# Kernel tuning notes

Hardware: AMD Instinct MI355X
Metric: run time of the kernel (lower is better)

Reference implementation:

```python
import jax, jax.numpy as jnp
import numpy as np

B, CIN, IMG = 8, 512, 112
P = IMG // 14          # patch_size = 8
NP = 14 * 14           # n_patch = 196
DEC, SKIP, EMB = 512, 512, 768
BN_EPS = 1e-3          # keras BatchNormalization default
IN_EPS = 1e-3          # tfa InstanceNormalization default


def conv2d(x, w, b, stride=1):
    # x: NCHW, w: OIHW
    y = jax.lax.conv_general_dilated(x, w, (stride, stride), 'VALID',
                                     dimension_numbers=('NCHW', 'OIHW', 'NCHW'))
    return y + b[None, :, None, None]


def bn_inf(x, g, b, m, v):
    scale = g / jnp.sqrt(v + BN_EPS)
    return (x - m[None, :, None, None]) * scale[None, :, None, None] + b[None, :, None, None]


def setup_inputs() -> dict:
    key = jax.random.key(0)
    ks = jax.random.split(key, 20)
    s = 0.05
    return {
        'decoder': jax.random.normal(ks[0], (B, CIN, IMG, IMG), jnp.float32),
        'trans': jax.random.normal(ks[1], (B, NP, EMB), jnp.float32),
        'pe_w': jax.random.normal(ks[2], (DEC, CIN, P, P), jnp.float32) * s,
        'pe_b': jax.random.normal(ks[3], (DEC,), jnp.float32) * s,
        'mc_w': jax.random.normal(ks[4], (SKIP, CIN, 1, 1), jnp.float32) * s,
        'mc_b': jax.random.normal(ks[5], (SKIP,), jnp.float32) * s,
        'bn1_g': jax.random.uniform(ks[6], (SKIP,), jnp.float32, 0.5, 1.5),
        'bn1_b': jax.random.normal(ks[7], (SKIP,), jnp.float32) * s,
        'bn1_m': jax.random.normal(ks[8], (SKIP,), jnp.float32) * s,
        'bn1_v': jax.random.uniform(ks[9], (SKIP,), jnp.float32, 0.5, 1.5),
        'wq': jax.random.normal(ks[10], (DEC, SKIP), jnp.float32) * s,
        'wk': jax.random.normal(ks[11], (EMB, SKIP), jnp.float32) * s,
        'wv': jax.random.normal(ks[12], (EMB, SKIP), jnp.float32) * s,
        'wo': jax.random.normal(ks[13], (SKIP, SKIP), jnp.float32) * s,
        'psi_g': jnp.ones((1,), jnp.float32),
        'psi_b': jnp.zeros((1,), jnp.float32),
        'rc_w': jax.random.normal(ks[14], (SKIP, SKIP, 1, 1), jnp.float32) * s,
        'rc_b': jax.random.normal(ks[15], (SKIP,), jnp.float32) * s,
        'bn2_g': jax.random.uniform(ks[16], (SKIP,), jnp.float32, 0.5, 1.5),
        'bn2_b': jax.random.normal(ks[17], (SKIP,), jnp.float32) * s,
        'bn2_m': jax.random.normal(ks[18], (SKIP,), jnp.float32) * s,
        'bn2_v': jax.random.uniform(ks[19], (SKIP,), jnp.float32, 0.5, 1.5),
    }


def reference(decoder, trans, pe_w, pe_b, mc_w, mc_b, bn1_g, bn1_b, bn1_m, bn1_v,
              wq, wk, wv, wo, psi_g, psi_b, rc_w, rc_b, bn2_g, bn2_b, bn2_m, bn2_v):
    # mask branch: 1x1 conv + BN + ReLU  -> [B, SKIP, IMG, IMG]
    mask = jax.nn.relu(bn_inf(conv2d(decoder, mc_w, mc_b), bn1_g, bn1_b, bn1_m, bn1_v))

    # patch embedding: strided conv -> [B, DEC, 14, 14] -> tokens [B, NP, DEC]
    dl = conv2d(decoder, pe_w, pe_b, stride=P)
    dl = dl.reshape(dl.shape[0], dl.shape[1], -1).transpose(0, 2, 1)

    q = jnp.einsum('bnd,ds->bsn', dl, wq)       # [B, SKIP, NP]
    k = jnp.einsum('bne,es->bns', trans, wk)    # [B, NP, SKIP]
    v = jnp.einsum('bne,es->bsn', trans, wv)    # [B, SKIP, NP]

    sim = jnp.einsum('bsn,bnt->bst', q, k)      # [B, SKIP, SKIP]
    # InstanceNorm over the (SKIP, SKIP) map per sample (single channel)
    mu = sim.mean(axis=(1, 2), keepdims=True)
    var = sim.var(axis=(1, 2), keepdims=True)
    sim = (sim - mu) / jnp.sqrt(var + IN_EPS) * psi_g[0] + psi_b[0]
    sim = jax.nn.softmax(sim, axis=-1)

    out = jnp.einsum('bst,btn->bns', sim, v)    # [B, NP, SKIP]
    out = jnp.einsum('bns,so->bno', out, wo)    # [B, NP, SKIP]

    # reconstruct: tokens -> [B, SKIP, 14, 14] -> nearest upsample x P -> 1x1 conv + BN + ReLU
    x = out.transpose(0, 2, 1).reshape(out.shape[0], SKIP, 14, 14)
    x = jnp.repeat(jnp.repeat(x, P, axis=2), P, axis=3)
    x = jax.nn.relu(bn_inf(conv2d(x, rc_w, rc_b), bn2_g, bn2_b, bn2_m, bn2_v))

    return x * mask
```

## Files before the change

kernel.cpp:

```cpp
#include <hip/hip_runtime.h>
#include <stdint.h>

typedef __attribute__((ext_vector_type(8))) short v8s;
typedef __attribute__((ext_vector_type(4))) float v4f;

__device__ __forceinline__ uint16_t f2bf(float x){
  uint32_t u = __float_as_uint(x);
  return (uint16_t)((u + 0x7FFFu + ((u >> 16) & 1u)) >> 16);
}
__device__ __forceinline__ uint32_t pk2(float a, float b){
  return (uint32_t)f2bf(a) | ((uint32_t)f2bf(b) << 16);
}

__device__ __forceinline__ void gl16(const uint16_t* g, uint16_t* l){
  __builtin_amdgcn_global_load_lds((const __attribute__((address_space(1))) void*)g,
                                   (__attribute__((address_space(3))) void*)l, 16, 0, 0);
}

__global__ void __launch_bounds__(256) dra_cvt(const float* __restrict__ s,
                                               uint16_t* __restrict__ d, int n8){
  int i = blockIdx.x * 256 + threadIdx.x;
  if (i >= n8) return;
  const float4* sp = (const float4*)(s + (size_t)i * 8);
  float4 f0 = sp[0], f1 = sp[1];
  uint4 u; u.x = pk2(f0.x, f0.y); u.y = pk2(f0.z, f0.w);
  u.z = pk2(f1.x, f1.y); u.w = pk2(f1.z, f1.w);
  *(uint4*)(d + (size_t)i * 8) = u;
}

__global__ void __launch_bounds__(256) dra_tcvt(const float* __restrict__ s,
                                                uint16_t* __restrict__ d, int R, int C){
  int r8 = R >> 3;
  int id = blockIdx.x * 256 + threadIdx.x;
  if (id >= C * r8) return;
  int c = id / r8, r0 = (id - c * r8) * 8;
  float v[8];
  #pragma unroll
  for (int e = 0; e < 8; e++) v[e] = s[(size_t)(r0 + e) * C + c];
  uint4 u; u.x = pk2(v[0], v[1]); u.y = pk2(v[2], v[3]);
  u.z = pk2(v[4], v[5]); u.w = pk2(v[6], v[7]);
  *(uint4*)(d + (size_t)c * R + r0) = u;
}

__global__ void __launch_bounds__(256) dra_tdec(const float* __restrict__ dec,
                                                uint16_t* __restrict__ decT){
  __shared__ uint16_t lt[64 * 80];
  int t = threadIdx.x;
  int pos0 = blockIdx.x * 64;
  int ci0  = blockIdx.y * 64;
  int b    = blockIdx.z;
  #pragma unroll
  for (int i = 0; i < 4; i++){
    int idx = t + i * 256;
    int ci_l = idx >> 4, p4 = (idx & 15) * 4;
    const float4 f = *(const float4*)(dec + ((size_t)(b * 512 + ci0 + ci_l)) * 12544 + pos0 + p4);
    lt[(p4 + 0) * 80 + ci_l] = f2bf(f.x);
    lt[(p4 + 1) * 80 + ci_l] = f2bf(f.y);
    lt[(p4 + 2) * 80 + ci_l] = f2bf(f.z);
    lt[(p4 + 3) * 80 + ci_l] = f2bf(f.w);
  }
  __syncthreads();
  #pragma unroll
  for (int i = 0; i < 2; i++){
    int idx = t + i * 256;
    int p_l = idx >> 3, u = idx & 7;
    uint4 v = *(const uint4*)&lt[p_l * 80 + u * 8];
    *(uint4*)(decT + ((size_t)b * 12544 + pos0 + p_l) * 512 + ci0 + u * 8) = v;
  }
}

__global__ void __launch_bounds__(256) dra_wpe2(const float* __restrict__ pw,
                                                uint16_t* __restrict__ w2){
  int id = blockIdx.x * 256 + threadIdx.x;
  if (id >= 2097152) return;
  int co = id >> 12, rem = id & 4095;
  int ci8 = rem >> 6, pix = rem & 63;
  const float* s = pw + (size_t)co * 32768 + ci8 * 512 + pix;
  float v[8];
  #pragma unroll
  for (int j = 0; j < 8; j++) v[j] = s[j * 64];
  uint4 u; u.x = pk2(v[0], v[1]); u.y = pk2(v[2], v[3]);
  u.z = pk2(v[4], v[5]); u.w = pk2(v[6], v[7]);
  *(uint4*)(w2 + (size_t)co * 32768 + pix * 512 + ci8 * 8) = u;
}

__global__ void __launch_bounds__(256) dra_transb(const float* __restrict__ tr,
                                                  uint16_t* __restrict__ d){
  int id = blockIdx.x * 256 + threadIdx.x;
  if (id >= 1792 * 96) return;
  int n = id / 96, e0 = (id - n * 96) * 8;
  int b = n / 224, nl = n - b * 224;
  uint4 u = {0u,0u,0u,0u};
  if (nl < 196){
    const float* sp = tr + ((size_t)(b * 196 + nl)) * 768 + e0;
    u.x = pk2(sp[0], sp[1]); u.y = pk2(sp[2], sp[3]);
    u.z = pk2(sp[4], sp[5]); u.w = pk2(sp[6], sp[7]);
  }
  *(uint4*)(d + (size_t)n * 768 + e0) = u;
}

__global__ void dra_scales(const float* mcb, const float* g1, const float* b1,
                           const float* m1, const float* v1,
                           const float* rcb, const float* g2, const float* b2,
                           const float* m2, const float* v2,
                           float* s1, float* o1, float* s2, float* o2){
  int i = blockIdx.x * 256 + threadIdx.x;
  if (i >= 512) return;
  float sc1 = g1[i] / sqrtf(v1[i] + 1e-3f);
  s1[i] = sc1; o1[i] = (mcb[i] - m1[i]) * sc1 + b1[i];
  float sc2 = g2[i] / sqrtf(v2[i] + 1e-3f);
  s2[i] = sc2; o2[i] = (rcb[i] - m2[i]) * sc2 + b2[i];
}

__global__ void __launch_bounds__(256, 4) dra_k1(const uint16_t* __restrict__ decT,
    const uint16_t* __restrict__ wpe2, float* __restrict__ part)
{
  __shared__ uint16_t lA[128 * 32];
  __shared__ uint16_t lB[128 * 32];
  int t = threadIdx.x;
  int L = blockIdx.x;
  int x = L & 7, n = L >> 3;
  int shi = n / 56, rem = n - shi * 56;
  int tok_t = rem >> 2, co_t = rem & 3;
  int s    = shi * 8 + x;
  int bco  = co_t * 128;
  int tok0 = tok_t * 128;
  int lane = t & 63, w = t >> 6;
  int wm = w >> 1, wn = w & 1;
  int lr = lane & 15, lg = lane >> 4;

  const uint16_t* aB[2]; const uint16_t* bB[2]; int uu[2];
  #pragma unroll
  for (int i = 0; i < 2; i++){
    int u = t + i * 256; uu[i] = u;
    int row = u >> 2, h = u & 3;
    int token = tok0 + row;
    int b = token / 224, tl = token - b * 224;
    if (tl > 195) tl = 195;
    int py = tl / 14, px = tl - py * 14;
    aB[i] = decT + ((size_t)b * 12544 + py * 896 + px * 8) * 512 + h * 8;
    bB[i] = wpe2 + (size_t)(bco + row) * 32768 + h * 8;
  }

  const v4f vzero = {0.f,0.f,0.f,0.f};
  v4f acc[4][4];
  #pragma unroll
  for (int i = 0; i < 4; i++)
    #pragma unroll
    for (int j = 0; j < 4; j++) acc[i][j] = vzero;

  for (int pix = s * 4; pix < s * 4 + 4; ++pix){
    int ky = pix >> 3, kx = pix & 7;
    int poff = (ky * 112 + kx) * 512;
    int k0p  = pix * 512;
    for (int ci0 = 0; ci0 < 512; ci0 += 32){
      gl16(aB[0] + poff + ci0, &lA[uu[0] * 8]);
      gl16(aB[1] + poff + ci0, &lA[uu[1] * 8]);
      gl16(bB[0] + k0p + ci0,  &lB[uu[0] * 8]);
      gl16(bB[1] + k0p + ci0,  &lB[uu[1] * 8]);
      __syncthreads();
      v8s av[4], bv[4];
      #pragma unroll
      for (int mf = 0; mf < 4; mf++) av[mf] = *(const v8s*)&lA[(wm*64 + mf*16 + lr) * 32 + lg * 8];
      #pragma unroll
      for (int nf = 0; nf < 4; nf++) bv[nf] = *(const v8s*)&lB[(wn*64 + nf*16 + lr) * 32 + lg * 8];
      #pragma unroll
      for (int mf = 0; mf < 4; mf++)
        #pragma unroll
        for (int nf = 0; nf < 4; nf++)
          acc[mf][nf] = __builtin_amdgcn_mfma_f32_16x16x32_bf16(av[mf], bv[nf], acc[mf][nf], 0, 0, 0);
      __syncthreads();
    }
  }
  float* pd = part + (size_t)s * 917504;
  #pragma unroll
  for (int mf = 0; mf < 4; mf++){
    #pragma unroll
    for (int nf = 0; nf < 4; nf++){
      int tokg = tok0 + wm*64 + mf*16 + lg*4;
      int cog  = bco  + wn*64 + nf*16 + lr;
      #pragma unroll
      for (int r = 0; r < 4; r++)
        pd[(size_t)(tokg + r) * 512 + cog] = acc[mf][nf][r];
    }
  }
}

__global__ void __launch_bounds__(256) dra_red(const float* __restrict__ part,
    const float* __restrict__ peb, uint16_t* __restrict__ dlb){
  int id = blockIdx.x * 256 + threadIdx.x;
  if (id >= 114688) return;
  int tok = id >> 6, c8 = (id & 63) * 8;
  float a0=0,a1=0,a2=0,a3=0,a4=0,a5=0,a6=0,a7=0;
  #pragma unroll
  for (int s = 0; s < 16; s++){
    const float* p = part + (size_t)s * 917504 + (size_t)tok * 512 + c8;
    float4 x = *(const float4*)p, y = *(const float4*)(p + 4);
    a0 += x.x; a1 += x.y; a2 += x.z; a3 += x.w;
    a4 += y.x; a5 += y.y; a6 += y.z; a7 += y.w;
  }
  const float4 b0 = *(const float4*)(peb + c8), b1 = *(const float4*)(peb + c8 + 4);
  uint4 o; o.x = pk2(a0 + b0.x, a1 + b0.y); o.y = pk2(a2 + b0.z, a3 + b0.w);
  o.z = pk2(a4 + b1.x, a5 + b1.y); o.w = pk2(a6 + b1.z, a7 + b1.w);
  *(uint4*)(dlb + (size_t)tok * 512 + c8) = o;
}

template<int MREP>
__global__ void __launch_bounds__(256, 2) dra_gemm(
    const uint16_t* __restrict__ A, const uint16_t* __restrict__ Bn, void* __restrict__ Dv,
    int M, int N, int K, int lda, int ldb, int ldd,
    long long sAz, long long sBz, long long sDz,
    int epi, const float* __restrict__ svec, const float* __restrict__ ovec)
{
  constexpr int BM = MREP * 32;
  __shared__ uint16_t lA[BM * 32];
  __shared__ uint16_t lB[64 * 32];
  int t = threadIdx.x, z = blockIdx.z;
  int bm = blockIdx.x * BM, bn = blockIdx.y * 64;
  const uint16_t* Az = A + (size_t)z * sAz;
  const uint16_t* Bz = Bn + (size_t)z * sBz;
  int lane = t & 63, w = t >> 6;
  int wm = w >> 1, wn = w & 1;
  int lr = lane & 15, lg = lane >> 4;

  const uint16_t* aSrc[MREP/2]; int uuA[MREP/2];
  #pragma unroll
  for (int i = 0; i < MREP/2; i++){
    int u = t + i * 256; uuA[i] = u;
    int row = u >> 2, c = u & 3;
    int cs = c ^ ((row >> 1) & 3);
    int rg = bm + row; if (rg >= M) rg = M - 1;
    aSrc[i] = Az + (size_t)rg * lda + cs * 8;
  }
  const uint16_t* bSrc;
  {
    int row = t >> 2, c = t & 3;
    int cs = c ^ ((row >> 1) & 3);
    bSrc = Bz + (size_t)(bn + row) * ldb + cs * 8;
  }

  int aoff[MREP], boff[2];
  #pragma unroll
  for (int mf = 0; mf < MREP; mf++){
    int R = wm*(MREP*16) + mf*16 + lr;
    aoff[mf] = R * 32 + (lg ^ ((R >> 1) & 3)) * 8;
  }
  #pragma unroll
  for (int nf = 0; nf < 2; nf++){
    int R = wn*32 + nf*16 + lr;
    boff[nf] = R * 32 + (lg ^ ((R >> 1) & 3)) * 8;
  }

  const v4f vzero = {0.f, 0.f, 0.f, 0.f};
  v4f acc[MREP][2];
  #pragma unroll
  for (int i = 0; i < MREP; i++){ acc[i][0] = vzero; acc[i][1] = vzero; }

  for (int k0 = 0; k0 < K; k0 += 32){
    #pragma unroll
    for (int i = 0; i < MREP/2; i++)
      gl16(aSrc[i] + k0, &lA[uuA[i] * 8]);
    gl16(bSrc + k0, &lB[t * 8]);
    __syncthreads();
    v8s av[MREP], bv[2];
    #pragma unroll
    for (int mf = 0; mf < MREP; mf++) av[mf] = *(const v8s*)&lA[aoff[mf]];
    #pragma unroll
    for (int nf = 0; nf < 2; nf++)    bv[nf] = *(const v8s*)&lB[boff[nf]];
    #pragma unroll
    for (int mf = 0; mf < MREP; mf++)
      #pragma unroll
      for (int nf = 0; nf < 2; nf++)
        acc[mf][nf] = __builtin_amdgcn_mfma_f32_16x16x32_bf16(av[mf], bv[nf], acc[mf][nf], 0, 0, 0);
    __syncthreads();
  }

  #pragma unroll
  for (int mf = 0; mf < MREP; mf++){
    #pragma unroll
    for (int nf = 0; nf < 2; nf++){
      int mg0 = bm + wm*(MREP*16) + mf*16 + lg*4;
      int ng  = bn + wn*32 + nf*16 + lr;
      #pragma unroll
      for (int r = 0; r < 4; r++){
        int mg = mg0 + r;
        if (mg < M){
          float val = acc[mf][nf][r];
          size_t di = (size_t)z * sDz + (size_t)mg * ldd + ng;
          if (epi == 0)      ((float*)Dv)[di] = val;
          else if (epi == 1) ((uint16_t*)Dv)[di] = f2bf(val);
          else ((float*)Dv)[di] = fmaxf(val * svec[mg] + ovec[mg], 0.f);
        }
      }
    }
  }
}

__global__ void __launch_bounds__(256) dra_stats1(const float* __restrict__ sim,
                                                  double* __restrict__ ps){
  __shared__ double d1[256], d2[256];
  int b = blockIdx.y, blk = blockIdx.x, t = threadIdx.x;
  const float* s = sim + (size_t)b * 262144 + (size_t)blk * 2048 + t * 8;
  float4 x = *(const float4*)s, y = *(const float4*)(s + 4);
  double p1 = (double)x.x + x.y + x.z + x.w + y.x + y.y + y.z + y.w;
  double p2 = (double)x.x*x.x + (double)x.y*x.y + (double)x.z*x.z + (double)x.w*x.w
            + (double)y.x*y.x + (double)y.y*y.y + (double)y.z*y.z + (double)y.w*y.w;
  d1[t] = p1; d2[t] = p2;
  __syncthreads();
  for (int o = 128; o > 0; o >>= 1){
    if (t < o){ d1[t] += d1[t + o]; d2[t] += d2[t + o]; }
    __syncthreads();
  }
  if (t == 0){
    ps[(b * 128 + blk) * 2 + 0] = d1[0];
    ps[(b * 128 + blk) * 2 + 1] = d2[0];
  }
}

__global__ void __launch_bounds__(128) dra_stats2(const double* __restrict__ ps,
    const float* __restrict__ psig, const float* __restrict__ psib, float* __restrict__ ac){
  __shared__ double d1[128], d2[128];
  int b = blockIdx.x, t = threadIdx.x;
  d1[t] = ps[(b * 128 + t) * 2 + 0];
  d2[t] = ps[(b * 128 + t) * 2 + 1];
  __syncthreads();
  for (int o = 64; o > 0; o >>= 1){
    if (t < o){ d1[t] += d1[t + o]; d2[t] += d2[t + o]; }
    __syncthreads();
  }
  if (t == 0){
    double mean = d1[0] * (1.0 / 262144.0);
    double var  = d2[0] * (1.0 / 262144.0) - mean * mean;
    float a = psig[0] / (float)sqrt(var + 1e-3);
    ac[b * 2 + 0] = a;
    ac[b * 2 + 1] = psib[0] - (float)mean * a;
  }
}

__global__ void __launch_bounds__(256) dra_soft(const float* __restrict__ sim,
    const float* __restrict__ ac, uint16_t* __restrict__ P){
  int srow = blockIdx.x, b = blockIdx.y, t = threadIdx.x;
  const float* row = sim + (size_t)b * 262144 + (size_t)srow * 512;
  float a = ac[b * 2], c = ac[b * 2 + 1];
  float v0 = row[t] * a + c, v1 = row[t + 256] * a + c;
  __shared__ float red[256];
  red[t] = fmaxf(v0, v1);
  __syncthreads();
  for (int o = 128; o > 0; o >>= 1){
    if (t < o) red[t] = fmaxf(red[t], red[t + o]);
    __syncthreads();
  }
  float m = red[0];
  __syncthreads();
  float e0 = __expf(v0 - m), e1 = __expf(v1 - m);
  red[t] = e0 + e1;
  __syncthreads();
  for (int o = 128; o > 0; o >>= 1){
    if (t < o) red[t] += red[t + o];
    __syncthreads();
  }
  float inv = 1.f / red[0];
  uint16_t* pr = P + (size_t)b * 262144 + (size_t)srow * 512;
  pr[t] = f2bf(e0 * inv); pr[t + 256] = f2bf(e1 * inv);
}

__global__ void __launch_bounds__(256, 4) dra_k3(const uint16_t* __restrict__ decT,
    const uint16_t* __restrict__ mcw, const float* __restrict__ s1,
    const float* __restrict__ o1, const float* __restrict__ recon,
    float* __restrict__ outp)
{
  __shared__ uint16_t lA[128 * 32];
  __shared__ uint16_t lB[128 * 32];
  int t = threadIdx.x;
  int L = blockIdx.x;
  int x = L & 7, n = L >> 3;
  int co_t = n & 3, pg = n >> 2;
  int p = pg * 8 + x;
  int bz = p / 98, pt = p - bz * 98;
  int bco  = co_t * 128;
  int pos0 = pt * 128;
  int lane = t & 63, w = t >> 6;
  int wm = w >> 1, wn = w & 1;
  int lr = lane & 15, lg = lane >> 4;

  const uint16_t* aB[2]; const uint16_t* bB[2]; int uu[2];
  #pragma unroll
  for (int i = 0; i < 2; i++){
    int u = t + i * 256; uu[i] = u;
    int row = u >> 2, h = u & 3;
    aB[i] = mcw  + (size_t)(bco + row) * 512 + h * 8;
    bB[i] = decT + ((size_t)bz * 12544 + pos0 + row) * 512 + h * 8;
  }

  const v4f vzero = {0.f,0.f,0.f,0.f};
  v4f acc[4][4];
  #pragma unroll
  for (int i = 0; i < 4; i++)
    #pragma unroll
    for (int j = 0; j < 4; j++) acc[i][j] = vzero;

  for (int k0 = 0; k0 < 512; k0 += 32){
    gl16(aB[0] + k0, &lA[uu[0] * 8]);
    gl16(aB[1] + k0, &lA[uu[1] * 8]);
    gl16(bB[0] + k0, &lB[uu[0] * 8]);
    gl16(bB[1] + k0, &lB[uu[1] * 8]);
    __syncthreads();
    v8s av[4], bv[4];
    #pragma unroll
    for (int mf = 0; mf < 4; mf++) av[mf] = *(const v8s*)&lA[(wm*64 + mf*16 + lr) * 32 + lg * 8];
    #pragma unroll
    for (int nf = 0; nf < 4; nf++) bv[nf] = *(const v8s*)&lB[(wn*64 + nf*16 + lr) * 32 + lg * 8];
    #pragma unroll
    for (int mf = 0; mf < 4; mf++)
      #pragma unroll
      for (int nf = 0; nf < 4; nf++)
        acc[mf][nf] = __builtin_amdgcn_mfma_f32_16x16x32_bf16(av[mf], bv[nf], acc[mf][nf], 0, 0, 0);
    __syncthreads();
  }

  #pragma unroll
  for (int mf = 0; mf < 4; mf++){
    #pragma unroll
    for (int r = 0; r < 4; r++){
      int co = bco + wm*64 + mf*16 + lg*4 + r;
      float sc = s1[co], of = o1[co];
      const float* rrow = recon + (size_t)co * 1792 + bz * 224;
      #pragma unroll
      for (int nf = 0; nf < 4; nf++){
        int pos = pos0 + wn*64 + nf*16 + lr;
        int h = pos / 112, wd = pos - h * 112;
        int pcol = (h >> 3) * 14 + (wd >> 3);
        float mask = fmaxf(acc[mf][nf][r] * sc + of, 0.f);
        outp[((size_t)(bz * 512 + co)) * 12544 + pos] = mask * rrow[pcol];
      }
    }
  }
}

extern "C" void kernel_launch(void* const* d_in, const int* in_sizes, int n_in,
                              void* d_out, int out_size, void* d_ws, size_t ws_size,
                              hipStream_t stream) {
  (void)in_sizes; (void)n_in; (void)out_size; (void)ws_size;
  const float* dec   = (const float*)d_in[0];
  const float* trans = (const float*)d_in[1];
  const float* pe_w  = (const float*)d_in[2];
  const float* pe_b  = (const float*)d_in[3];
  const float* mc_w  = (const float*)d_in[4];
  const float* mc_b  = (const float*)d_in[5];
  const float* bn1g  = (const float*)d_in[6];
  const float* bn1b  = (const float*)d_in[7];
  const float* bn1m  = (const float*)d_in[8];
  const float* bn1v  = (const float*)d_in[9];
  const float* wq    = (const float*)d_in[10];
  const float* wk    = (const float*)d_in[11];
  const float* wv    = (const float*)d_in[12];
  const float* wo    = (const float*)d_in[13];
  const float* psig  = (const float*)d_in[14];
  const float* psib  = (const float*)d_in[15];
  const float* rc_w  = (const float*)d_in[16];
  const float* rc_b  = (const float*)d_in[17];
  const float* bn2g  = (const float*)d_in[18];
  const float* bn2b  = (const float*)d_in[19];
  const float* bn2m  = (const float*)d_in[20];
  const float* bn2v  = (const float*)d_in[21];

  char* p = (char*)d_ws;
  auto take = [&](size_t bytes) -> void* {
    void* r = (void*)p; p += (bytes + 255) & ~(size_t)255; return r;
  };
  uint16_t* decT   = (uint16_t*)take((size_t)8 * 12544 * 512 * 2);
  uint16_t* wpe2   = (uint16_t*)take((size_t)512 * 32768 * 2);
  uint16_t* mcw    = (uint16_t*)take((size_t)512 * 512 * 2);
  uint16_t* rcw    = (uint16_t*)take((size_t)512 * 512 * 2);
  uint16_t* wqT    = (uint16_t*)take((size_t)512 * 512 * 2);
  uint16_t* woT    = (uint16_t*)take((size_t)512 * 512 * 2);
  uint16_t* wkT    = (uint16_t*)take((size_t)512 * 768 * 2);
  uint16_t* wvT    = (uint16_t*)take((size_t)512 * 768 * 2);
  uint16_t* transb = (uint16_t*)take((size_t)1792 * 768 * 2);
  float*    s1v    = (float*)take(512 * 4);
  float*    o1v    = (float*)take(512 * 4);
  float*    s2v    = (float*)take(512 * 4);
  float*    o2v    = (float*)take(512 * 4);
  uint16_t* dlb    = (uint16_t*)take((size_t)1792 * 512 * 2);
  uint16_t* Qt     = (uint16_t*)take((size_t)512 * 1792 * 2);
  uint16_t* Kt     = (uint16_t*)take((size_t)512 * 1792 * 2);
  uint16_t* Vb     = (uint16_t*)take((size_t)1792 * 512 * 2);
  float*    ac     = (float*)take(256);
  double*   ps     = (double*)take((size_t)8 * 128 * 2 * 8);
  float*    part   = (float*)take((size_t)16 * 1792 * 512 * 4);
  float*    simb   = part;
  uint16_t* P      = (uint16_t*)(part + 2097152);
  uint16_t* outb   = P + 2097152;
  uint16_t* out2   = outb + 917504;
  float*    recon  = (float*)(out2 + 917504);

  dra_tdec<<<dim3(196, 8, 8), 256, 0, stream>>>(dec, decT);
  dra_wpe2<<<8192, 256, 0, stream>>>(pe_w, wpe2);
  dra_cvt<<<128, 256, 0, stream>>>(mc_w, mcw, 32768);
  dra_cvt<<<128, 256, 0, stream>>>(rc_w, rcw, 32768);
  dra_tcvt<<<128, 256, 0, stream>>>(wq, wqT, 512, 512);
  dra_tcvt<<<192, 256, 0, stream>>>(wk, wkT, 768, 512);
  dra_tcvt<<<192, 256, 0, stream>>>(wv, wvT, 768, 512);
  dra_tcvt<<<128, 256, 0, stream>>>(wo, woT, 512, 512);
  dra_transb<<<672, 256, 0, stream>>>(trans, transb);
  dra_scales<<<2, 256, 0, stream>>>(mc_b, bn1g, bn1b, bn1m, bn1v,
                                    rc_b, bn2g, bn2b, bn2m, bn2v, s1v, o1v, s2v, o2v);

  dra_k1<<<896, 256, 0, stream>>>(decT, wpe2, part);
  dra_red<<<448, 256, 0, stream>>>(part, pe_b, dlb);

  dra_gemm<2><<<dim3(8, 28, 1), 256, 0, stream>>>(wqT, dlb, Qt, 512, 1792, 512,
      512, 512, 1792, 0, 0, 0, 1, nullptr, nullptr);
  dra_gemm<2><<<dim3(8, 28, 1), 256, 0, stream>>>(wkT, transb, Kt, 512, 1792, 768,
      768, 768, 1792, 0, 0, 0, 1, nullptr, nullptr);
  dra_gemm<2><<<dim3(28, 8, 1), 256, 0, stream>>>(transb, wvT, Vb, 1792, 512, 768,
      768, 768, 512, 0, 0, 0, 1, nullptr, nullptr);

  dra_gemm<2><<<dim3(8, 8, 8), 256, 0, stream>>>(Qt, Kt, simb, 512, 512, 224,
      1792, 1792, 512, 224, 224, 262144, 0, nullptr, nullptr);
  dra_stats1<<<dim3(128, 8), 256, 0, stream>>>(simb, ps);
  dra_stats2<<<8, 128, 0, stream>>>(ps, psig, psib, ac);
  dra_soft<<<dim3(512, 8), 256, 0, stream>>>(simb, ac, P);

  dra_gemm<2><<<dim3(4, 8, 8), 256, 0, stream>>>(Vb, P, outb, 224, 512, 512,
      512, 512, 512, 114688, 262144, 114688, 1, nullptr, nullptr);
  dra_gemm<2><<<dim3(28, 8, 1), 256, 0, stream>>>(outb, woT, out2, 1792, 512, 512,
      512, 512, 512, 0, 0, 0, 1, nullptr, nullptr);
  dra_gemm<2><<<dim3(8, 28, 1), 256, 0, stream>>>(rcw, out2, recon, 512, 1792, 512,
      512, 512, 1792, 0, 0, 0, 2, s2v, o2v);

  dra_k3<<<3136, 256, 0, stream>>>(decT, mcw, s1v, o1v, recon, (float*)d_out);
}
```

Before: 427.4 us.

## Triple-buffer LDS pipeline with register-prefetched weights and XOR swizzle in k1/k3

```diff
diff --git a/kernel.cpp b/kernel.cpp
--- a/kernel.cpp
+++ b/kernel.cpp
@@ -112,11 +112,10 @@
   s2[i] = sc2; o2[i] = (rcb[i] - m2[i]) * sc2 + b2[i];
 }
 
-__global__ void __launch_bounds__(256, 4) dra_k1(const uint16_t* __restrict__ decT,
+__global__ void __launch_bounds__(256, 3) dra_k1(const uint16_t* __restrict__ decT,
     const uint16_t* __restrict__ wpe2, float* __restrict__ part)
 {
-  __shared__ uint16_t lA[128 * 32];
-  __shared__ uint16_t lB[128 * 32];
+  __shared__ uint16_t lA[3][128 * 32];
   int t = threadIdx.x;
   int L = blockIdx.x;
   int x = L & 7, n = L >> 3;
@@ -129,17 +128,28 @@
   int wm = w >> 1, wn = w & 1;
   int lr = lane & 15, lg = lane >> 4;
 
-  const uint16_t* aB[2]; const uint16_t* bB[2]; int uu[2];
+  const uint16_t* aB[2];
   #pragma unroll
   for (int i = 0; i < 2; i++){
-    int u = t + i * 256; uu[i] = u;
+    int u = t + i * 256;
     int row = u >> 2, h = u & 3;
+    int hs = h ^ ((row >> 1) & 3);
     int token = tok0 + row;
     int b = token / 224, tl = token - b * 224;
     if (tl > 195) tl = 195;
     int py = tl / 14, px = tl - py * 14;
-    aB[i] = decT + ((size_t)b * 12544 + py * 896 + px * 8) * 512 + h * 8;
-    bB[i] = wpe2 + (size_t)(bco + row) * 32768 + h * 8;
+    aB[i] = decT + ((size_t)b * 12544 + py * 896 + px * 8) * 512 + hs * 8;
+  }
+  const uint16_t* bP[4];
+  #pragma unroll
+  for (int nf = 0; nf < 4; nf++)
+    bP[nf] = wpe2 + (size_t)(bco + wn*64 + nf*16 + lr) * 32768 + s * 2048 + lg * 8;
+
+  int aoff[4];
+  #pragma unroll
+  for (int mf = 0; mf < 4; mf++){
+    int R = wm*64 + mf*16 + lr;
+    aoff[mf] = R * 32 + (lg ^ ((R >> 1) & 3)) * 8;
   }
 
   const v4f vzero = {0.f,0.f,0.f,0.f};
@@ -149,29 +159,52 @@
     #pragma unroll
     for (int j = 0; j < 4; j++) acc[i][j] = vzero;
 
-  for (int pix = s * 4; pix < s * 4 + 4; ++pix){
-    int ky = pix >> 3, kx = pix & 7;
-    int poff = (ky * 112 + kx) * 512;
-    int k0p  = pix * 512;
-    for (int ci0 = 0; ci0 < 512; ci0 += 32){
-      gl16(aB[0] + poff + ci0, &lA[uu[0] * 8]);
-      gl16(aB[1] + poff + ci0, &lA[uu[1] * 8]);
-      gl16(bB[0] + k0p + ci0,  &lB[uu[0] * 8]);
-      gl16(bB[1] + k0p + ci0,  &lB[uu[1] * 8]);
-      __syncthreads();
-      v8s av[4], bv[4];
+  auto stageA = [&](int kk){
+    int pix = s * 4 + (kk >> 4);
+    int base = ((pix >> 3) * 112 + (pix & 7)) * 512 + ((kk & 15) << 5);
+    int pb = kk % 3;
+    gl16(aB[0] + base, &lA[pb][t * 8]);
+    gl16(aB[1] + base, &lA[pb][(t + 256) * 8]);
+  };
+  v8s bpf0[4], bpf1[4];
+  auto loadB = [&](int kk, v8s (&bp)[4]){
+    int ko = kk << 5;
+    #pragma unroll
+    for (int nf = 0; nf < 4; nf++) bp[nf] = *(const v8s*)(bP[nf] + ko);
+  };
+
+  stageA(0); loadB(0, bpf0);
+  stageA(1); loadB(1, bpf1);
+  __builtin_amdgcn_sched_barrier(0);
+  asm volatile("s_waitcnt vmcnt(6)" ::: "memory");
+  __builtin_amdgcn_s_barrier();
+  __builtin_amdgcn_sched_barrier(0);
+
+  auto sub = [&](int kk, v8s (&bp)[4]){
+    v8s av[4], bv[4];
+    #pragma unroll
+    for (int mf = 0; mf < 4; mf++) av[mf] = *(const v8s*)&lA[kk % 3][aoff[mf]];
+    #pragma unroll
+    for (int nf = 0; nf < 4; nf++) bv[nf] = bp[nf];
+    #pragma unroll
+    for (int mf = 0; mf < 4; mf++)
       #pragma unroll
-      for (int mf = 0; mf < 4; mf++) av[mf] = *(const v8s*)&lA[(wm*64 + mf*16 + lr) * 32 + lg * 8];
-      #pragma unroll
-      for (int nf = 0; nf < 4; nf++) bv[nf] = *(const v8s*)&lB[(wn*64 + nf*16 + lr) * 32 + lg * 8];
-      #pragma unroll
-      for (int mf = 0; mf < 4; mf++)
-        #pragma unroll
-        for (int nf = 0; nf < 4; nf++)
-          acc[mf][nf] = __builtin_amdgcn_mfma_f32_16x16x32_bf16(av[mf], bv[nf], acc[mf][nf], 0, 0, 0);
-      __syncthreads();
+      for (int nf = 0; nf < 4; nf++)
+        acc[mf][nf] = __builtin_amdgcn_mfma_f32_16x16x32_bf16(av[mf], bv[nf], acc[mf][nf], 0, 0, 0);
+    if (kk + 2 < 64){ stageA(kk + 2); loadB(kk + 2, bp); }
+    __builtin_amdgcn_sched_barrier(0);
+    if (kk < 63){
+      if (kk < 62) asm volatile("s_waitcnt vmcnt(6)" ::: "memory");
+      else         asm volatile("s_waitcnt vmcnt(0)" ::: "memory");
+      __builtin_amdgcn_s_barrier();
+      __builtin_amdgcn_sched_barrier(0);
     }
-  }
+  };
+  for (int kk2 = 0; kk2 < 64; kk2 += 2){
+    sub(kk2,     bpf0);
+    sub(kk2 + 1, bpf1);
+  }
+
   float* pd = part + (size_t)s * 917504;
   #pragma unroll
   for (int mf = 0; mf < 4; mf++){
@@ -364,13 +397,12 @@
   pr[t] = f2bf(e0 * inv); pr[t + 256] = f2bf(e1 * inv);
 }
 
-__global__ void __launch_bounds__(256, 4) dra_k3(const uint16_t* __restrict__ decT,
+__global__ void __launch_bounds__(256, 3) dra_k3(const uint16_t* __restrict__ decT,
     const uint16_t* __restrict__ mcw, const float* __restrict__ s1,
     const float* __restrict__ o1, const float* __restrict__ recon,
     float* __restrict__ outp)
 {
-  __shared__ uint16_t lA[128 * 32];
-  __shared__ uint16_t lB[128 * 32];
+  __shared__ uint16_t lB[3][128 * 32];
   int t = threadIdx.x;
   int L = blockIdx.x;
   int x = L & 7, n = L >> 3;
@@ -383,13 +415,24 @@
   int wm = w >> 1, wn = w & 1;
   int lr = lane & 15, lg = lane >> 4;
 
-  const uint16_t* aB[2]; const uint16_t* bB[2]; int uu[2];
+  const uint16_t* bB[2];
   #pragma unroll
   for (int i = 0; i < 2; i++){
-    int u = t + i * 256; uu[i] = u;
+    int u = t + i * 256;
     int row = u >> 2, h = u & 3;
-    aB[i] = mcw  + (size_t)(bco + row) * 512 + h * 8;
-    bB[i] = decT + ((size_t)bz * 12544 + pos0 + row) * 512 + h * 8;
+    int hs = h ^ ((row >> 1) & 3);
+    bB[i] = decT + ((size_t)bz * 12544 + pos0 + row) * 512 + hs * 8;
+  }
+  const uint16_t* aP[4];
+  #pragma unroll
+  for (int mf = 0; mf < 4; mf++)
+    aP[mf] = mcw + (size_t)(bco + wm*64 + mf*16 + lr) * 512 + lg * 8;
+
+  int boff[4];
+  #pragma unroll
+  for (int nf = 0; nf < 4; nf++){
+    int R = wn*64 + nf*16 + lr;
+    boff[nf] = R * 32 + (lg ^ ((R >> 1) & 3)) * 8;
   }
 
   const v4f vzero = {0.f,0.f,0.f,0.f};
@@ -399,23 +442,49 @@
     #pragma unroll
     for (int j = 0; j < 4; j++) acc[i][j] = vzero;
 
-  for (int k0 = 0; k0 < 512; k0 += 32){
-    gl16(aB[0] + k0, &lA[uu[0] * 8]);
-    gl16(aB[1] + k0, &lA[uu[1] * 8]);
-    gl16(bB[0] + k0, &lB[uu[0] * 8]);
-    gl16(bB[1] + k0, &lB[uu[1] * 8]);
-    __syncthreads();
+  auto stageB = [&](int kk){
+    int ko = kk << 5, pb = kk % 3;
+    gl16(bB[0] + ko, &lB[pb][t * 8]);
+    gl16(bB[1] + ko, &lB[pb][(t + 256) * 8]);
+  };
+  v8s apf0[4], apf1[4];
+  auto loadA = [&](int kk, v8s (&ap)[4]){
+    int ko = kk << 5;
+    #pragma unroll
+    for (int mf = 0; mf < 4; mf++) ap[mf] = *(const v8s*)(aP[mf] + ko);
+  };
+
+  stageB(0); loadA(0, apf0);
+  stageB(1); loadA(1, apf1);
+  __builtin_amdgcn_sched_barrier(0);
+  asm volatile("s_waitcnt vmcnt(6)" ::: "memory");
+  __builtin_amdgcn_s_barrier();
+  __builtin_amdgcn_sched_barrier(0);
+
+  auto sub = [&](int kk, v8s (&ap)[4]){
     v8s av[4], bv[4];
     #pragma unroll
-    for (int mf = 0; mf < 4; mf++) av[mf] = *(const v8s*)&lA[(wm*64 + mf*16 + lr) * 32 + lg * 8];
-    #pragma unroll
-    for (int nf = 0; nf < 4; nf++) bv[nf] = *(const v8s*)&lB[(wn*64 + nf*16 + lr) * 32 + lg * 8];
+    for (int mf = 0; mf < 4; mf++) av[mf] = ap[mf];
+    #pragma unroll
+    for (int nf = 0; nf < 4; nf++) bv[nf] = *(const v8s*)&lB[kk % 3][boff[nf]];
     #pragma unroll
     for (int mf = 0; mf < 4; mf++)
       #pragma unroll
       for (int nf = 0; nf < 4; nf++)
         acc[mf][nf] = __builtin_amdgcn_mfma_f32_16x16x32_bf16(av[mf], bv[nf], acc[mf][nf], 0, 0, 0);
-    __syncthreads();
+    if (kk + 2 < 16){ stageB(kk + 2); loadA(kk + 2, ap); }
+    __builtin_amdgcn_sched_barrier(0);
+    if (kk < 15){
+      if (kk < 14) asm volatile("s_waitcnt vmcnt(6)" ::: "memory");
+      else         asm volatile("s_waitcnt vmcnt(0)" ::: "memory");
+      __builtin_amdgcn_s_barrier();
+      __builtin_amdgcn_sched_barrier(0);
+    }
+  };
+  #pragma unroll
+  for (int kk2 = 0; kk2 < 16; kk2 += 2){
+    sub(kk2,     apf0);
+    sub(kk2 + 1, apf1);
   }
 
   #pragma unroll
```

New measurement: 517.6 us. 1.21x slower.
